# Optimization experiments

Hardware: AMD Instinct MI355X
Metric: run time of the kernel (lower is better)

The kernel has to match this reference:

```python
import jax, jax.numpy as jnp
import numpy as np

B, S, E, H = 4, 2048, 1024, 4
D = E // H  # head_dim = 256


def setup_inputs() -> dict:
    key = jax.random.key(0)
    ks = jax.random.split(key, 9)
    scale = 1.0 / np.sqrt(E)
    return {
        "hidden_states": jax.random.normal(ks[0], (B, S, E), jnp.float32),
        "Wq": jax.random.normal(ks[1], (E, E), jnp.float32) * scale,
        "Wk": jax.random.normal(ks[2], (E, E), jnp.float32) * scale,
        "Wv": jax.random.normal(ks[3], (E, E), jnp.float32) * scale,
        "Wo": jax.random.normal(ks[4], (E, E), jnp.float32) * scale,
        "bo": jax.random.normal(ks[5], (E,), jnp.float32) * 0.02,
        "betas": jax.random.normal(ks[6], (1, H, 1, 1), jnp.float32),
        "mem": jax.random.uniform(ks[7], (H, D, D), jnp.float32),
        "z": jax.random.uniform(ks[8], (H, D, 1), jnp.float32),
    }


def _split_heads(t):  # [B,S,E] -> [B,H,S,D]
    return t.reshape(B, S, H, D).transpose(0, 2, 1, 3)


def reference(hidden_states, Wq, Wk, Wv, Wo, bo, betas, mem, z):
    q = _split_heads(hidden_states @ Wq)  # [B,H,S,D]
    k = _split_heads(hidden_states @ Wk)
    v = _split_heads(hidden_states @ Wv)

    # linear-attention feature map (ELU + 1)
    sigma_q = jax.nn.elu(q) + 1.0
    sigma_k = jax.nn.elu(k) + 1.0

    # compressive-memory read: mem [H,D,D], z [H,D,1] broadcast over batch
    A_mem = (sigma_q @ mem) / (sigma_q @ z + 1e-6)  # [B,H,S,D]

    # standard causal softmax attention
    attn_weights = jnp.einsum("bhqd,bhkd->bhqk", q, k)
    causal = jnp.tril(jnp.ones((S, S), bool))
    mask_value = jnp.finfo(attn_weights.dtype).min
    attn_weights = jnp.where(causal, attn_weights, mask_value)
    attn_weights = jax.nn.softmax(attn_weights, axis=-1)
    attn_output = jnp.einsum("bhqk,bhkd->bhqd", attn_weights, v)

    # per-head sigmoid gate mixing memory read and local attention
    gate = jax.nn.sigmoid(betas)  # [1,H,1,1]
    attn_output = gate * A_mem + (1.0 - gate) * attn_output

    # memory update (delta rule)
    delta = (sigma_k @ mem) / (sigma_k @ z + 1e-6)  # [B,H,S,D]
    mem_new = mem + jnp.einsum("bhsd,bhse->bhde", sigma_k, v - delta)  # [B,H,D,D]
    z_new = z + sigma_k.sum(axis=-2, keepdims=True).transpose(0, 1, 3, 2)  # [B,H,D,1]

    out = attn_output.transpose(0, 2, 1, 3).reshape(B, S, E) @ Wo + bo
    return out, mem_new, z_new
```

## Files before the change

kernel.cpp:

```cpp
#include <hip/hip_runtime.h>
#include <math.h>

#define Bn 4
#define Sn 2048
#define En 1024
#define Hn 4
#define Dn 256

typedef _Float16 half8 __attribute__((ext_vector_type(8)));
typedef _Float16 half4v __attribute__((ext_vector_type(4)));
typedef float floatx4 __attribute__((ext_vector_type(4)));

#define MFMA16(a, b, c) __builtin_amdgcn_mfma_f32_16x16x32_f16((a), (b), (c), 0, 0, 0)

__device__ __forceinline__ float elup1(float x) {
    return x > 0.0f ? x + 1.0f : __expf(x);
}

__global__ __launch_bounds__(256) void trans_f32f16_k(
    const float* __restrict__ src, _Float16* __restrict__ dst, int R, int C) {
    __shared__ float T[64][65];
    const int tid = threadIdx.x;
    const int c0 = blockIdx.x * 64, r0 = blockIdx.y * 64;
    src += (size_t)blockIdx.z * R * C;
    dst += (size_t)blockIdx.z * R * C;
    {
        const int tr = tid >> 2, tc = (tid & 3) * 16;
        const float* s = src + (size_t)(r0 + tr) * C + c0 + tc;
        #pragma unroll
        for (int i = 0; i < 4; ++i) {
            float4 v = *(const float4*)(s + i * 4);
            T[tr][tc + i * 4 + 0] = v.x;
            T[tr][tc + i * 4 + 1] = v.y;
            T[tr][tc + i * 4 + 2] = v.z;
            T[tr][tc + i * 4 + 3] = v.w;
        }
    }
    __syncthreads();
    {
        const int cr = tid >> 2, rc = (tid & 3) * 16;
        half8 h0, h1;
        #pragma unroll
        for (int i = 0; i < 8; ++i) h0[i] = (_Float16)T[rc + i][cr];
        #pragma unroll
        for (int i = 0; i < 8; ++i) h1[i] = (_Float16)T[rc + 8 + i][cr];
        _Float16* d = dst + (size_t)(c0 + cr) * R + r0 + rc;
        *(half8*)d = h0;
        *(half8*)(d + 8) = h1;
    }
}

__global__ __launch_bounds__(256) void trans_h16_k(
    const _Float16* __restrict__ Vh, _Float16* __restrict__ Vtg) {
    __shared__ __align__(16) unsigned short T[64 * 72];
    const int tid = threadIdx.x;
    const int s0 = blockIdx.x * 64;
    const int e0 = blockIdx.y * 64;
    const int b = blockIdx.z;
    const int h = e0 >> 8, d0 = e0 & 255;
    {
        const int tr = tid >> 2, tc = (tid & 3) * 16;
        const _Float16* s = Vh + (size_t)(b * Sn + s0 + tr) * En + e0 + tc;
        _Float16* d = (_Float16*)T + tr * 72 + tc;
        *(half8*)d = *(const half8*)s;
        *(half8*)(d + 8) = *(const half8*)(s + 8);
    }
    __syncthreads();
    {
        const int dr = tid >> 2, sc = (tid & 3) * 16;
        const _Float16* Tp = (const _Float16*)T;
        half8 h0, h1;
        #pragma unroll
        for (int i = 0; i < 8; ++i) h0[i] = Tp[(sc + i) * 72 + dr];
        #pragma unroll
        for (int i = 0; i < 8; ++i) h1[i] = Tp[(sc + 8 + i) * 72 + dr];
        _Float16* d = Vtg + (size_t)((b * 4 + h) * 256 + d0 + dr) * (size_t)Sn + s0 + sc;
        *(half8*)d = h0;
        *(half8*)(d + 8) = h1;
    }
}

template <bool A32>
__global__ __launch_bounds__(256) void gemm16_k(
    const void* __restrict__ Ap, const _Float16* __restrict__ Bt,
    _Float16* __restrict__ C16, float* __restrict__ C32,
    const float* __restrict__ bias) {
    __shared__ __align__(16) unsigned short Ah[128 * 40];
    __shared__ __align__(16) unsigned short Bh[128 * 40];
    const int tid = threadIdx.x;
    const int lane = tid & 63, w = tid >> 6, quad = lane >> 4, l15 = lane & 15;
    const int bm = blockIdx.y * 128, bn = blockIdx.x * 128;
    floatx4 acc[2][8];
    #pragma unroll
    for (int mt = 0; mt < 2; ++mt)
        #pragma unroll
        for (int nt = 0; nt < 8; ++nt) acc[mt][nt] = (floatx4){0.f, 0.f, 0.f, 0.f};

    const int srow = tid >> 1, skoff = (tid & 1) * 16;
    const _Float16* bs = Bt + (size_t)(bn + srow) * 1024 + skoff;
    _Float16* ad = (_Float16*)Ah + srow * 40 + skoff;
    _Float16* bd = (_Float16*)Bh + srow * 40 + skoff;

    for (int k0 = 0; k0 < 1024; k0 += 32) {
        if (k0) __syncthreads();
        if constexpr (A32) {
            const float* as = (const float*)Ap + (size_t)(bm + srow) * 1024 + skoff + k0;
            half8 h0, h1;
            #pragma unroll
            for (int i = 0; i < 2; ++i) {
                float4 f0 = *(const float4*)(as + i * 8);
                float4 f1 = *(const float4*)(as + i * 8 + 4);
                half8* hp = i ? &h1 : &h0;
                (*hp)[0] = (_Float16)f0.x; (*hp)[1] = (_Float16)f0.y;
                (*hp)[2] = (_Float16)f0.z; (*hp)[3] = (_Float16)f0.w;
                (*hp)[4] = (_Float16)f1.x; (*hp)[5] = (_Float16)f1.y;
                (*hp)[6] = (_Float16)f1.z; (*hp)[7] = (_Float16)f1.w;
            }
            *(half8*)ad = h0;
            *(half8*)(ad + 8) = h1;
        } else {
            const _Float16* as = (const _Float16*)Ap + (size_t)(bm + srow) * 1024 + skoff + k0;
            *(half8*)ad = *(const half8*)as;
            *(half8*)(ad + 8) = *(const half8*)(as + 8);
        }
        *(half8*)bd = *(const half8*)(bs + k0);
        *(half8*)(bd + 8) = *(const half8*)(bs + k0 + 8);
        __syncthreads();
        half8 af0 = *(const half8*)((const _Float16*)Ah + (w * 32 + l15) * 40 + quad * 8);
        half8 af1 = *(const half8*)((const _Float16*)Ah + (w * 32 + 16 + l15) * 40 + quad * 8);
        #pragma unroll
        for (int nt = 0; nt < 8; ++nt) {
            half8 bf = *(const half8*)((const _Float16*)Bh + (nt * 16 + l15) * 40 + quad * 8);
            acc[0][nt] = MFMA16(af0, bf, acc[0][nt]);
            acc[1][nt] = MFMA16(af1, bf, acc[1][nt]);
        }
    }
    #pragma unroll
    for (int mt = 0; mt < 2; ++mt)
        #pragma unroll
        for (int nt = 0; nt < 8; ++nt)
            #pragma unroll
            for (int r = 0; r < 4; ++r) {
                const int row = bm + w * 32 + mt * 16 + quad * 4 + r;
                const int col = bn + nt * 16 + l15;
                if (C16)
                    C16[(size_t)row * 1024 + col] = (_Float16)acc[mt][nt][r];
                else
                    C32[(size_t)row * 1024 + col] = acc[mt][nt][r] + bias[col];
            }
}

__global__ __launch_bounds__(256, 3) void flash_gate_k(
    const _Float16* __restrict__ Qh, const _Float16* __restrict__ Khg,
    const _Float16* __restrict__ Vtg, const _Float16* __restrict__ memT,
    const float* __restrict__ zp, const float* __restrict__ betas,
    _Float16* __restrict__ Cmb, _Float16* __restrict__ Opart,
    float* __restrict__ mpart, float* __restrict__ lpart) {
    __shared__ __align__(16) unsigned short Ksh[32 * 264];
    __shared__ __align__(16) unsigned short Vt[256 * 40];
    __shared__ __align__(16) unsigned short Pb[64 * 40];

    const int tid = threadIdx.x;
    const int lane = tid & 63;
    const int w = tid >> 6;
    const int quad = lane >> 4;
    const int l15 = lane & 15;
    const int bx = blockIdx.x;
    const int bh = blockIdx.y;
    const int b = bh >> 2, h = bh & 3;

    int qt, kt0, kt1, unit;
    if (bx < 32) {
        qt = 31 - (bx >> 1);
        unit = bx & 1;
        kt0 = unit ? (qt + 1) : 0;
        kt1 = unit ? (2 * qt + 2) : (qt + 1);
    } else {
        qt = 15 - (bx - 32);
        unit = 0;
        kt0 = 0;
        kt1 = 2 * qt + 2;
    }
    const bool two = (bx < 32);
    const int q0 = qt * 64;

    const _Float16* Qrow = Qh + (size_t)(b * Sn + q0 + w * 16 + l15) * En + h * Dn;
    half8 qf[8];
    #pragma unroll
    for (int kc = 0; kc < 8; ++kc) qf[kc] = *(const half8*)(Qrow + kc * 32 + quad * 8);

    floatx4 acc[16];
    #pragma unroll
    for (int nt = 0; nt < 16; ++nt) acc[nt] = (floatx4){0.f, 0.f, 0.f, 0.f};

    const float gate = 1.0f / (1.0f + __expf(-betas[h]));
    const float omg = 1.0f - gate;
    _Float16* Cb = Cmb + (size_t)(b * Sn + q0 + w * 16) * En + h * Dn;
    _Float16* KshF = (_Float16*)Ksh;
    _Float16* VtF = (_Float16*)Vt;
    _Float16* PbF = (_Float16*)Pb;

    if (unit == 0) {
        float denp = 0.0f;
        const _Float16* memh = memT + (size_t)h * Dn * Dn;
        for (int dc = 0; dc < 8; ++dc) {
            __syncthreads();
            {
                const _Float16* src = memh + (size_t)tid * 256 + dc * 32;
                _Float16* dst = VtF + tid * 40;
                #pragma unroll
                for (int u = 0; u < 4; ++u) *(half8*)(dst + u * 8) = *(const half8*)(src + u * 8);
            }
            __syncthreads();
            half8 sv;
            const float* zb = zp + h * Dn + dc * 32 + quad * 8;
            #pragma unroll
            for (int j = 0; j < 8; ++j) {
                const float s = elup1((float)qf[dc][j]);
                sv[j] = (_Float16)s;
                denp += s * zb[j];
            }
            #pragma unroll
            for (int nt = 0; nt < 16; ++nt) {
                half8 bm = *(const half8*)(VtF + (nt * 16 + l15) * 40 + quad * 8);
                acc[nt] = MFMA16(sv, bm, acc[nt]);
            }
        }
        denp += __shfl_xor(denp, 16);
        denp += __shfl_xor(denp, 32);
        const float deninv = 1.0f / (denp + 1e-6f);
        float den4[4];
        #pragma unroll
        for (int r = 0; r < 4; ++r) den4[r] = __shfl(deninv, quad * 4 + r);
        #pragma unroll
        for (int nt = 0; nt < 16; ++nt)
            #pragma unroll
            for (int r = 0; r < 4; ++r) {
                Cb[(size_t)(quad * 4 + r) * En + nt * 16 + l15] =
                    (_Float16)(gate * acc[nt][r] * den4[r]);
                acc[nt][r] = 0.0f;
            }
    }

    const _Float16* Kbase = Khg + (size_t)(b * Sn) * En + h * Dn;
    const _Float16* Vtb = Vtg + (size_t)bh * 256 * (size_t)Sn;
    const _Float16* kptr = Kbase + (size_t)(kt0 * 32 + (tid >> 3)) * En + (tid & 7) * 32;
    const _Float16* vptr = Vtb + (size_t)tid * Sn + kt0 * 32;
    half8 kr[4], vr[4];
    #pragma unroll
    for (int u = 0; u < 4; ++u) {
        kr[u] = *(const half8*)(kptr + u * 8);
        vr[u] = *(const half8*)(vptr + u * 8);
    }

    float mold[4] = {-1e30f, -1e30f, -1e30f, -1e30f};
    float lsum[4] = {0.f, 0.f, 0.f, 0.f};
    float alpha[4];
    const int krow_off = (tid >> 3) * 264 + (tid & 7) * 32;

    for (int kt = kt0; kt < kt1; ++kt) {
        const int k0 = kt * 32;
        __syncthreads();
        #pragma unroll
        for (int u = 0; u < 4; ++u) {
            *(half8*)(KshF + krow_off + u * 8) = kr[u];
            *(half8*)(VtF + tid * 40 + u * 8) = vr[u];
        }
        __syncthreads();
        if (kt + 1 < kt1) {
            kptr += 32 * En;
            vptr += 32;
            #pragma unroll
            for (int u = 0; u < 4; ++u) {
                kr[u] = *(const half8*)(kptr + u * 8);
                vr[u] = *(const half8*)(vptr + u * 8);
            }
        }

        floatx4 S0 = (floatx4){0.f, 0.f, 0.f, 0.f};
        floatx4 S1 = (floatx4){0.f, 0.f, 0.f, 0.f};
        #pragma unroll
        for (int kc = 0; kc < 8; ++kc) {
            half8 kf0 = *(const half8*)(KshF + l15 * 264 + kc * 32 + quad * 8);
            half8 kf1 = *(const half8*)(KshF + (16 + l15) * 264 + kc * 32 + quad * 8);
            S0 = MFMA16(qf[kc], kf0, S0);
            S1 = MFMA16(qf[kc], kf1, S1);
        }
        if (kt >= 2 * qt) {
            #pragma unroll
            for (int r = 0; r < 4; ++r) {
                const int qg = q0 + w * 16 + quad * 4 + r;
                if (k0 + l15 > qg) S0[r] = -1e30f;
                if (k0 + 16 + l15 > qg) S1[r] = -1e30f;
            }
        }
        #pragma unroll
        for (int r = 0; r < 4; ++r) {
            float mx = fmaxf(S0[r], S1[r]);
            mx = fmaxf(mx, __shfl_xor(mx, 1));
            mx = fmaxf(mx, __shfl_xor(mx, 2));
            mx = fmaxf(mx, __shfl_xor(mx, 4));
            mx = fmaxf(mx, __shfl_xor(mx, 8));
            const float mnew = fmaxf(mold[r], mx);
            alpha[r] = __expf(mold[r] - mnew);
            mold[r] = mnew;
            const float p0 = __expf(S0[r] - mnew);
            const float p1 = __expf(S1[r] - mnew);
            float ps = p0 + p1;
            ps += __shfl_xor(ps, 1);
            ps += __shfl_xor(ps, 2);
            ps += __shfl_xor(ps, 4);
            ps += __shfl_xor(ps, 8);
            lsum[r] = lsum[r] * alpha[r] + ps;
            _Float16* pr = PbF + (w * 16 + quad * 4 + r) * 40;
            pr[l15] = (_Float16)p0;
            pr[16 + l15] = (_Float16)p1;
        }
        #pragma unroll
        for (int nt = 0; nt < 16; ++nt) {
            acc[nt][0] *= alpha[0];
            acc[nt][1] *= alpha[1];
            acc[nt][2] *= alpha[2];
            acc[nt][3] *= alpha[3];
        }
        __asm__ volatile("s_waitcnt lgkmcnt(0)" ::: "memory");
        half8 pf = *(const half8*)(PbF + (w * 16 + l15) * 40 + quad * 8);
        #pragma unroll
        for (int nt = 0; nt < 16; ++nt) {
            half8 vf = *(const half8*)(VtF + (nt * 16 + l15) * 40 + quad * 8);
            acc[nt] = MFMA16(pf, vf, acc[nt]);
        }
    }

    if (!two) {
        #pragma unroll
        for (int r = 0; r < 4; ++r) alpha[r] = omg / lsum[r];
        #pragma unroll
        for (int nt = 0; nt < 16; ++nt)
            #pragma unroll
            for (int r = 0; r < 4; ++r) {
                const size_t idx = (size_t)(quad * 4 + r) * En + nt * 16 + l15;
                Cb[idx] = (_Float16)((float)Cb[idx] + acc[nt][r] * alpha[r]);
            }
    } else {
        const int pidx = ((qt - 16) * 16 + bh) * 2 + unit;
        _Float16* Op = Opart + ((size_t)pidx * 64 + w * 16) * 256;
        #pragma unroll
        for (int nt = 0; nt < 16; ++nt)
            #pragma unroll
            for (int r = 0; r < 4; ++r)
                Op[(quad * 4 + r) * 256 + nt * 16 + l15] = (_Float16)acc[nt][r];
        if (l15 == 0) {
            #pragma unroll
            for (int r = 0; r < 4; ++r) {
                mpart[pidx * 64 + w * 16 + quad * 4 + r] = mold[r];
                lpart[pidx * 64 + w * 16 + quad * 4 + r] = lsum[r];
            }
        }
    }
}

__global__ __launch_bounds__(256) void merge_k(
    const _Float16* __restrict__ Opart, const float* __restrict__ mpart,
    const float* __restrict__ lpart, const float* __restrict__ betas,
    _Float16* __restrict__ Cmb) {
    const int qi = blockIdx.x;
    const int bh = blockIdx.y;
    const int b = bh >> 2, h = bh & 3;
    const int tid = threadIdx.x;
    const int idx = (qi * 16 + bh) * 2;
    const float gate = 1.0f / (1.0f + __expf(-betas[h]));
    const float omg = 1.0f - gate;
    const int rsub = tid >> 6;
    const int c0 = (tid & 63) * 4;
    const _Float16* O0 = Opart + (size_t)idx * 64 * 256;
    const _Float16* O1 = O0 + 64 * 256;
    const int q0 = (16 + qi) * 64;
    for (int chunk = 0; chunk < 16; ++chunk) {
        const int r = chunk * 4 + rsub;
        const float m0 = mpart[idx * 64 + r], l0 = lpart[idx * 64 + r];
        const float m1 = mpart[(idx + 1) * 64 + r], l1 = lpart[(idx + 1) * 64 + r];
        const float mm = fmaxf(m0, m1);
        const float s0 = __expf(m0 - mm), s1 = __expf(m1 - mm);
        const float rl = omg / (l0 * s0 + l1 * s1);
        half4v o0 = *(const half4v*)(O0 + r * 256 + c0);
        half4v o1 = *(const half4v*)(O1 + r * 256 + c0);
        _Float16* cp = Cmb + (size_t)(b * Sn + q0 + r) * En + h * Dn + c0;
        half4v cv = *(half4v*)cp;
        #pragma unroll
        for (int j = 0; j < 4; ++j)
            cv[j] = (_Float16)((float)cv[j] + ((float)o0[j] * s0 + (float)o1[j] * s1) * rl);
        *(half4v*)cp = cv;
    }
}

__global__ __launch_bounds__(256) void delta_v_k(
    const _Float16* __restrict__ Kg, _Float16* __restrict__ Vg,
    const float* __restrict__ memp, const float* __restrict__ zp) {
    __shared__ float SK[32][256];
    __shared__ float rden[32];
    const int tid = threadIdx.x;
    const int st = blockIdx.x;
    const int h = blockIdx.y;
    const int b = blockIdx.z;
    const int s0 = st * 32;
    const _Float16* Kb = Kg + (size_t)(b * Sn + s0) * En + h * Dn;
    _Float16* Vb = Vg + (size_t)(b * Sn + s0) * En + h * Dn;
    const float* memh = memp + (size_t)h * Dn * Dn;
    const float* zh = zp + (size_t)h * Dn;

    {
        const int lr = tid >> 3, ld = (tid & 7) * 32;
        const _Float16* kr = Kb + (size_t)lr * En + ld;
        #pragma unroll
        for (int u = 0; u < 4; ++u) {
            half8 k8 = *(const half8*)(kr + u * 8);
            #pragma unroll
            for (int j = 0; j < 8; ++j) SK[lr][ld + u * 8 + j] = elup1((float)k8[j]);
        }
    }
    __syncthreads();
    {
        const int r = tid >> 3;
        const int sl = (tid & 7) << 5;
        float part = 0.0f;
        #pragma unroll 8
        for (int d = 0; d < 32; ++d) part += SK[r][sl + d] * zh[sl + d];
        part += __shfl_down(part, 4);
        part += __shfl_down(part, 2);
        part += __shfl_down(part, 1);
        if ((tid & 7) == 0) rden[r] = 1.0f / (part + 1e-6f);
    }
    __syncthreads();
    const int c0 = (tid & 63) << 2;
    const int rb = tid >> 6;
    float dl[8][4] = {};
    for (int kk = 0; kk < Dn; ++kk) {
        const float4 m4 = *(const float4*)(memh + (size_t)kk * Dn + c0);
        #pragma unroll
        for (int k = 0; k < 8; ++k) {
            const float sk = SK[rb + 4 * k][kk];
            dl[k][0] += sk * m4.x;
            dl[k][1] += sk * m4.y;
            dl[k][2] += sk * m4.z;
            dl[k][3] += sk * m4.w;
        }
    }
    #pragma unroll
    for (int k = 0; k < 8; ++k) {
        const int r = rb + 4 * k;
        const float rd = rden[r];
        _Float16* vp = Vb + (size_t)r * En + c0;
        half4v v4 = *(half4v*)vp;
        #pragma unroll
        for (int j = 0; j < 4; ++j) v4[j] = (_Float16)((float)v4[j] - dl[k][j] * rd);
        *(half4v*)vp = v4;
    }
}

__global__ __launch_bounds__(256) void mem_update_k(
    const _Float16* __restrict__ Kg, const _Float16* __restrict__ U,
    const float* __restrict__ memp, float* __restrict__ mem_new) {
    __shared__ float As[16][64];
    __shared__ float Bs[16][64];
    const int tid = threadIdx.x;
    const int bn = blockIdx.x * 64;
    const int bm = blockIdx.y * 64;
    const int bh = blockIdx.z;
    const int b = bh >> 2;
    const int h = bh & 3;
    const _Float16* Kb = Kg + (size_t)b * Sn * En + h * Dn;
    const _Float16* Ub = U + (size_t)b * Sn * En + h * Dn;
    const int tr = tid >> 4, tc = tid & 15;
    const int lr = tid >> 4;
    const int lc = (tid & 15) << 2;
    float acc[4][4] = {};
    for (int s0 = 0; s0 < Sn; s0 += 16) {
        half4v a4 = *(const half4v*)(Kb + (size_t)(s0 + lr) * En + bm + lc);
        As[lr][lc + 0] = elup1((float)a4[0]);
        As[lr][lc + 1] = elup1((float)a4[1]);
        As[lr][lc + 2] = elup1((float)a4[2]);
        As[lr][lc + 3] = elup1((float)a4[3]);
        half4v b4 = *(const half4v*)(Ub + (size_t)(s0 + lr) * En + bn + lc);
        Bs[lr][lc + 0] = (float)b4[0];
        Bs[lr][lc + 1] = (float)b4[1];
        Bs[lr][lc + 2] = (float)b4[2];
        Bs[lr][lc + 3] = (float)b4[3];
        __syncthreads();
        #pragma unroll
        for (int kk = 0; kk < 16; ++kk) {
            float a[4], bb[4];
            #pragma unroll
            for (int i = 0; i < 4; ++i) a[i] = As[kk][tr * 4 + i];
            #pragma unroll
            for (int j = 0; j < 4; ++j) bb[j] = Bs[kk][tc * 4 + j];
            #pragma unroll
            for (int i = 0; i < 4; ++i)
                #pragma unroll
                for (int j = 0; j < 4; ++j)
                    acc[i][j] += a[i] * bb[j];
        }
        __syncthreads();
    }
    const float* memh = memp + (size_t)h * Dn * Dn;
    float* mout = mem_new + (size_t)bh * Dn * Dn;
    #pragma unroll
    for (int i = 0; i < 4; ++i) {
        const int dm = bm + tr * 4 + i;
        const float4 m4 = *(const float4*)(memh + (size_t)dm * Dn + bn + tc * 4);
        float4 r;
        r.x = m4.x + acc[i][0];
        r.y = m4.y + acc[i][1];
        r.z = m4.z + acc[i][2];
        r.w = m4.w + acc[i][3];
        *(float4*)(mout + (size_t)dm * Dn + bn + tc * 4) = r;
    }
}

__global__ __launch_bounds__(256) void znew_init_k(
    const float* __restrict__ zp, float* __restrict__ z_new) {
    const int bh = blockIdx.x;
    const int h = bh & 3;
    z_new[(size_t)bh * Dn + threadIdx.x] = zp[(size_t)h * Dn + threadIdx.x];
}

__global__ __launch_bounds__(256) void znew_acc_k(
    const _Float16* __restrict__ Kg, float* __restrict__ z_new) {
    const int bh = blockIdx.y;
    const int b = bh >> 2;
    const int h = bh & 3;
    const int s0 = blockIdx.x * 256;
    const _Float16* Kb = Kg + (size_t)(b * Sn + s0) * En + h * Dn;
    float acc = 0.0f;
    for (int s = 0; s < 256; ++s) acc += elup1((float)Kb[(size_t)s * En + threadIdx.x]);
    atomicAdd(&z_new[(size_t)bh * Dn + threadIdx.x], acc);
}

extern "C" void kernel_launch(void* const* d_in, const int* in_sizes, int n_in,
                              void* d_out, int out_size, void* d_ws, size_t ws_size,
                              hipStream_t stream) {
    const float* hidden = (const float*)d_in[0];
    const float* Wq = (const float*)d_in[1];
    const float* Wk = (const float*)d_in[2];
    const float* Wv = (const float*)d_in[3];
    const float* Wo = (const float*)d_in[4];
    const float* bo = (const float*)d_in[5];
    const float* betas = (const float*)d_in[6];
    const float* memp = (const float*)d_in[7];
    const float* zp = (const float*)d_in[8];

    float* out = (float*)d_out;
    float* mem_new = out + (size_t)Bn * Sn * En;
    float* z_new = mem_new + (size_t)Bn * Hn * Dn * Dn;

    const size_t BSE = (size_t)Bn * Sn * En;
    _Float16* p = (_Float16*)d_ws;
    _Float16* Qh = p;    p += BSE;
    _Float16* Kh = p;    p += BSE;
    _Float16* Vh = p;    p += BSE;
    _Float16* Vtg = p;   p += BSE;
    _Float16* Cmb = p;   p += BSE;
    _Float16* Opart = p; p += (size_t)512 * 64 * 256;
    _Float16* WqT = p;   p += (size_t)En * En;
    _Float16* WkT = p;   p += (size_t)En * En;
    _Float16* WvT = p;   p += (size_t)En * En;
    _Float16* WoT = p;   p += (size_t)En * En;
    _Float16* memT = p;  p += (size_t)Hn * Dn * Dn;
    float* fp = (float*)p;
    float* mpart = fp;   fp += 512 * 64;
    float* lpart = fp;   fp += 512 * 64;

    trans_f32f16_k<<<dim3(16, 16, 1), 256, 0, stream>>>(Wq, WqT, En, En);
    trans_f32f16_k<<<dim3(16, 16, 1), 256, 0, stream>>>(Wk, WkT, En, En);
    trans_f32f16_k<<<dim3(16, 16, 1), 256, 0, stream>>>(Wv, WvT, En, En);
    trans_f32f16_k<<<dim3(16, 16, 1), 256, 0, stream>>>(Wo, WoT, En, En);
    trans_f32f16_k<<<dim3(4, 4, 4), 256, 0, stream>>>(memp, memT, Dn, Dn);

    gemm16_k<true><<<dim3(8, 64), 256, 0, stream>>>(hidden, WqT, Qh, nullptr, nullptr);
    gemm16_k<true><<<dim3(8, 64), 256, 0, stream>>>(hidden, WkT, Kh, nullptr, nullptr);
    gemm16_k<true><<<dim3(8, 64), 256, 0, stream>>>(hidden, WvT, Vh, nullptr, nullptr);

    trans_h16_k<<<dim3(32, 16, 4), 256, 0, stream>>>(Vh, Vtg);

    flash_gate_k<<<dim3(48, 16), 256, 0, stream>>>(
        Qh, Kh, Vtg, memT, zp, betas, Cmb, Opart, mpart, lpart);
    merge_k<<<dim3(16, 16), 256, 0, stream>>>(Opart, mpart, lpart, betas, Cmb);

    delta_v_k<<<dim3(64, 4, 4), 256, 0, stream>>>(Kh, Vh, memp, zp);
    mem_update_k<<<dim3(4, 4, 16), 256, 0, stream>>>(Kh, Vh, memp, mem_new);

    znew_init_k<<<16, 256, 0, stream>>>(zp, z_new);
    znew_acc_k<<<dim3(8, 16), 256, 0, stream>>>(Kh, z_new);

    gemm16_k<false><<<dim3(8, 64), 256, 0, stream>>>(Cmb, WoT, nullptr, out, bo);
}
```

Before: 651.5 us.

## Fuse QKV GEMM, move delta/memory update to MFMA, drop LDS staging in flash kernel

The hidden state is converted to fp16 once, and a single fused QKV GEMM with 64x64 warp tiles and a K-step of 64 scatters its output into Q, K and V. The flash kernel now reads K, V and mem fragments straight from global memory instead of staging them in LDS. It computes the row sum through an extra MFMA against a ones vector and skips the rescale when the running max does not change. The scalar fp32 delta-rule and memory-update kernels are replaced by MFMA kernels working on transposed sigma_k and V-minus-delta buffers. Uncoalesced direct global reads in the attention loop could increase memory latency.

Result: slower. 711.4 us (+9.2%).

```diff
diff --git a/kernel.cpp b/kernel.cpp
--- a/kernel.cpp
+++ b/kernel.cpp
@@ -15,6 +15,18 @@
 
 __device__ __forceinline__ float elup1(float x) {
     return x > 0.0f ? x + 1.0f : __expf(x);
+}
+
+__global__ void cvt_h_k(const float* __restrict__ src, _Float16* __restrict__ dst, int n4) {
+    int idx = blockIdx.x * 256 + threadIdx.x;
+    const int stride = gridDim.x * 256;
+    for (; idx < n4; idx += stride) {
+        float4 v = ((const float4*)src)[idx];
+        half4v o;
+        o[0] = (_Float16)v.x; o[1] = (_Float16)v.y;
+        o[2] = (_Float16)v.z; o[3] = (_Float16)v.w;
+        ((half4v*)dst)[idx] = o;
+    }
 }
 
 __global__ __launch_bounds__(256) void trans_f32f16_k(
@@ -80,73 +92,70 @@
     }
 }
 
-template <bool A32>
-__global__ __launch_bounds__(256) void gemm16_k(
-    const void* __restrict__ Ap, const _Float16* __restrict__ Bt,
-    _Float16* __restrict__ C16, float* __restrict__ C32,
-    const float* __restrict__ bias) {
-    __shared__ __align__(16) unsigned short Ah[128 * 40];
-    __shared__ __align__(16) unsigned short Bh[128 * 40];
+template <bool OUT32>
+__global__ __launch_bounds__(256) void gemm_fused_k(
+    const _Float16* __restrict__ A, const _Float16* __restrict__ Bt,
+    _Float16* __restrict__ Qo, _Float16* __restrict__ Ko, _Float16* __restrict__ Vo,
+    float* __restrict__ C32, const float* __restrict__ bias) {
+    __shared__ __align__(16) unsigned short Ah[128 * 72];
+    __shared__ __align__(16) unsigned short Bh[128 * 72];
     const int tid = threadIdx.x;
     const int lane = tid & 63, w = tid >> 6, quad = lane >> 4, l15 = lane & 15;
     const int bm = blockIdx.y * 128, bn = blockIdx.x * 128;
-    floatx4 acc[2][8];
-    #pragma unroll
-    for (int mt = 0; mt < 2; ++mt)
-        #pragma unroll
-        for (int nt = 0; nt < 8; ++nt) acc[mt][nt] = (floatx4){0.f, 0.f, 0.f, 0.f};
-
-    const int srow = tid >> 1, skoff = (tid & 1) * 16;
+    const int wr = (w >> 1) * 64, wc = (w & 1) * 64;
+    floatx4 acc[4][4];
+    #pragma unroll
+    for (int mt = 0; mt < 4; ++mt)
+        #pragma unroll
+        for (int nt = 0; nt < 4; ++nt) acc[mt][nt] = (floatx4){0.f, 0.f, 0.f, 0.f};
+
+    const int srow = tid >> 1, skoff = (tid & 1) * 32;
+    const _Float16* as = A + (size_t)(bm + srow) * 1024 + skoff;
     const _Float16* bs = Bt + (size_t)(bn + srow) * 1024 + skoff;
-    _Float16* ad = (_Float16*)Ah + srow * 40 + skoff;
-    _Float16* bd = (_Float16*)Bh + srow * 40 + skoff;
-
-    for (int k0 = 0; k0 < 1024; k0 += 32) {
+    _Float16* ad = (_Float16*)Ah + srow * 72 + skoff;
+    _Float16* bd = (_Float16*)Bh + srow * 72 + skoff;
+    const _Float16* AhF = (const _Float16*)Ah;
+    const _Float16* BhF = (const _Float16*)Bh;
+
+    for (int k0 = 0; k0 < 1024; k0 += 64) {
         if (k0) __syncthreads();
-        if constexpr (A32) {
-            const float* as = (const float*)Ap + (size_t)(bm + srow) * 1024 + skoff + k0;
-            half8 h0, h1;
-            #pragma unroll
-            for (int i = 0; i < 2; ++i) {
-                float4 f0 = *(const float4*)(as + i * 8);
-                float4 f1 = *(const float4*)(as + i * 8 + 4);
-                half8* hp = i ? &h1 : &h0;
-                (*hp)[0] = (_Float16)f0.x; (*hp)[1] = (_Float16)f0.y;
-                (*hp)[2] = (_Float16)f0.z; (*hp)[3] = (_Float16)f0.w;
-                (*hp)[4] = (_Float16)f1.x; (*hp)[5] = (_Float16)f1.y;
-                (*hp)[6] = (_Float16)f1.z; (*hp)[7] = (_Float16)f1.w;
-            }
-            *(half8*)ad = h0;
-            *(half8*)(ad + 8) = h1;
-        } else {
-            const _Float16* as = (const _Float16*)Ap + (size_t)(bm + srow) * 1024 + skoff + k0;
-            *(half8*)ad = *(const half8*)as;
-            *(half8*)(ad + 8) = *(const half8*)(as + 8);
-        }
-        *(half8*)bd = *(const half8*)(bs + k0);
-        *(half8*)(bd + 8) = *(const half8*)(bs + k0 + 8);
+        #pragma unroll
+        for (int u = 0; u < 4; ++u) {
+            *(half8*)(ad + u * 8) = *(const half8*)(as + k0 + u * 8);
+            *(half8*)(bd + u * 8) = *(const half8*)(bs + k0 + u * 8);
+        }
         __syncthreads();
-        half8 af0 = *(const half8*)((const _Float16*)Ah + (w * 32 + l15) * 40 + quad * 8);
-        half8 af1 = *(const half8*)((const _Float16*)Ah + (w * 32 + 16 + l15) * 40 + quad * 8);
-        #pragma unroll
-        for (int nt = 0; nt < 8; ++nt) {
-            half8 bf = *(const half8*)((const _Float16*)Bh + (nt * 16 + l15) * 40 + quad * 8);
-            acc[0][nt] = MFMA16(af0, bf, acc[0][nt]);
-            acc[1][nt] = MFMA16(af1, bf, acc[1][nt]);
-        }
-    }
-    #pragma unroll
-    for (int mt = 0; mt < 2; ++mt)
-        #pragma unroll
-        for (int nt = 0; nt < 8; ++nt)
+        #pragma unroll
+        for (int ks = 0; ks < 2; ++ks) {
+            half8 af[4], bf[4];
+            #pragma unroll
+            for (int mt = 0; mt < 4; ++mt)
+                af[mt] = *(const half8*)(AhF + (wr + mt * 16 + l15) * 72 + ks * 32 + quad * 8);
+            #pragma unroll
+            for (int nt = 0; nt < 4; ++nt)
+                bf[nt] = *(const half8*)(BhF + (wc + nt * 16 + l15) * 72 + ks * 32 + quad * 8);
+            #pragma unroll
+            for (int mt = 0; mt < 4; ++mt)
+                #pragma unroll
+                for (int nt = 0; nt < 4; ++nt)
+                    acc[mt][nt] = MFMA16(af[mt], bf[nt], acc[mt][nt]);
+        }
+    }
+    #pragma unroll
+    for (int mt = 0; mt < 4; ++mt)
+        #pragma unroll
+        for (int nt = 0; nt < 4; ++nt)
             #pragma unroll
             for (int r = 0; r < 4; ++r) {
-                const int row = bm + w * 32 + mt * 16 + quad * 4 + r;
-                const int col = bn + nt * 16 + l15;
-                if (C16)
-                    C16[(size_t)row * 1024 + col] = (_Float16)acc[mt][nt][r];
-                else
+                const int row = bm + wr + mt * 16 + quad * 4 + r;
+                const int col = bn + wc + nt * 16 + l15;
+                if constexpr (OUT32) {
                     C32[(size_t)row * 1024 + col] = acc[mt][nt][r] + bias[col];
+                } else {
+                    const int m = col >> 10, c = col & 1023;
+                    _Float16* dst = (m == 0) ? Qo : ((m == 1) ? Ko : Vo);
+                    dst[(size_t)row * 1024 + c] = (_Float16)acc[mt][nt][r];
+                }
             }
 }
 
@@ -156,17 +165,11 @@
     const float* __restrict__ zp, const float* __restrict__ betas,
     _Float16* __restrict__ Cmb, _Float16* __restrict__ Opart,
     float* __restrict__ mpart, float* __restrict__ lpart) {
-    __shared__ __align__(16) unsigned short Ksh[32 * 264];
-    __shared__ __align__(16) unsigned short Vt[256 * 40];
-    __shared__ __align__(16) unsigned short Pb[64 * 40];
-
+    __shared__ __align__(16) unsigned short Pb[4 * 16 * 40];
     const int tid = threadIdx.x;
     const int lane = tid & 63;
-    const int w = tid >> 6;
-    const int quad = lane >> 4;
-    const int l15 = lane & 15;
-    const int bx = blockIdx.x;
-    const int bh = blockIdx.y;
+    const int w = tid >> 6, quad = lane >> 4, l15 = lane & 15;
+    const int bx = blockIdx.x, bh = blockIdx.y;
     const int b = bh >> 2, h = bh & 3;
 
     int qt, kt0, kt1, unit;
@@ -189,29 +192,22 @@
     #pragma unroll
     for (int kc = 0; kc < 8; ++kc) qf[kc] = *(const half8*)(Qrow + kc * 32 + quad * 8);
 
-    floatx4 acc[16];
-    #pragma unroll
-    for (int nt = 0; nt < 16; ++nt) acc[nt] = (floatx4){0.f, 0.f, 0.f, 0.f};
+    floatx4 acc[17];
+    #pragma unroll
+    for (int nt = 0; nt < 17; ++nt) acc[nt] = (floatx4){0.f, 0.f, 0.f, 0.f};
+    half8 ones;
+    #pragma unroll
+    for (int j = 0; j < 8; ++j) ones[j] = (_Float16)1.0f;
 
     const float gate = 1.0f / (1.0f + __expf(-betas[h]));
     const float omg = 1.0f - gate;
     _Float16* Cb = Cmb + (size_t)(b * Sn + q0 + w * 16) * En + h * Dn;
-    _Float16* KshF = (_Float16*)Ksh;
-    _Float16* VtF = (_Float16*)Vt;
     _Float16* PbF = (_Float16*)Pb;
 
     if (unit == 0) {
         float denp = 0.0f;
-        const _Float16* memh = memT + (size_t)h * Dn * Dn;
+        const _Float16* memh = memT + (size_t)h * Dn * Dn + (size_t)l15 * Dn + quad * 8;
         for (int dc = 0; dc < 8; ++dc) {
-            __syncthreads();
-            {
-                const _Float16* src = memh + (size_t)tid * 256 + dc * 32;
-                _Float16* dst = VtF + tid * 40;
-                #pragma unroll
-                for (int u = 0; u < 4; ++u) *(half8*)(dst + u * 8) = *(const half8*)(src + u * 8);
-            }
-            __syncthreads();
             half8 sv;
             const float* zb = zp + h * Dn + dc * 32 + quad * 8;
             #pragma unroll
@@ -222,8 +218,8 @@
             }
             #pragma unroll
             for (int nt = 0; nt < 16; ++nt) {
-                half8 bm = *(const half8*)(VtF + (nt * 16 + l15) * 40 + quad * 8);
-                acc[nt] = MFMA16(sv, bm, acc[nt]);
+                half8 bmf = *(const half8*)(memh + (size_t)(nt * 16) * Dn + dc * 32);
+                acc[nt] = MFMA16(sv, bmf, acc[nt]);
             }
         }
         denp += __shfl_xor(denp, 16);
@@ -242,51 +238,25 @@
             }
     }
 
-    const _Float16* Kbase = Khg + (size_t)(b * Sn) * En + h * Dn;
-    const _Float16* Vtb = Vtg + (size_t)bh * 256 * (size_t)Sn;
-    const _Float16* kptr = Kbase + (size_t)(kt0 * 32 + (tid >> 3)) * En + (tid & 7) * 32;
-    const _Float16* vptr = Vtb + (size_t)tid * Sn + kt0 * 32;
-    half8 kr[4], vr[4];
-    #pragma unroll
-    for (int u = 0; u < 4; ++u) {
-        kr[u] = *(const half8*)(kptr + u * 8);
-        vr[u] = *(const half8*)(vptr + u * 8);
-    }
-
+    const _Float16* kb0 = Khg + (size_t)(b * Sn + kt0 * 32 + l15) * En + h * Dn + quad * 8;
+    const _Float16* kb1 = kb0 + (size_t)16 * En;
+    const _Float16* vb = Vtg + (size_t)(bh * 256 + l15) * Sn + kt0 * 32 + quad * 8;
     float mold[4] = {-1e30f, -1e30f, -1e30f, -1e30f};
-    float lsum[4] = {0.f, 0.f, 0.f, 0.f};
-    float alpha[4];
-    const int krow_off = (tid >> 3) * 264 + (tid & 7) * 32;
 
     for (int kt = kt0; kt < kt1; ++kt) {
-        const int k0 = kt * 32;
-        __syncthreads();
-        #pragma unroll
-        for (int u = 0; u < 4; ++u) {
-            *(half8*)(KshF + krow_off + u * 8) = kr[u];
-            *(half8*)(VtF + tid * 40 + u * 8) = vr[u];
-        }
-        __syncthreads();
-        if (kt + 1 < kt1) {
-            kptr += 32 * En;
-            vptr += 32;
-            #pragma unroll
-            for (int u = 0; u < 4; ++u) {
-                kr[u] = *(const half8*)(kptr + u * 8);
-                vr[u] = *(const half8*)(vptr + u * 8);
-            }
-        }
-
         floatx4 S0 = (floatx4){0.f, 0.f, 0.f, 0.f};
         floatx4 S1 = (floatx4){0.f, 0.f, 0.f, 0.f};
         #pragma unroll
         for (int kc = 0; kc < 8; ++kc) {
-            half8 kf0 = *(const half8*)(KshF + l15 * 264 + kc * 32 + quad * 8);
-            half8 kf1 = *(const half8*)(KshF + (16 + l15) * 264 + kc * 32 + quad * 8);
+            half8 kf0 = *(const half8*)(kb0 + kc * 32);
+            half8 kf1 = *(const half8*)(kb1 + kc * 32);
             S0 = MFMA16(qf[kc], kf0, S0);
             S1 = MFMA16(qf[kc], kf1, S1);
         }
+        kb0 += (size_t)32 * En;
+        kb1 += (size_t)32 * En;
         if (kt >= 2 * qt) {
+            const int k0 = kt * 32;
             #pragma unroll
             for (int r = 0; r < 4; ++r) {
                 const int qg = q0 + w * 16 + quad * 4 + r;
@@ -294,6 +264,8 @@
                 if (k0 + 16 + l15 > qg) S1[r] = -1e30f;
             }
         }
+        float alpha[4];
+        bool nr = true;
         #pragma unroll
         for (int r = 0; r < 4; ++r) {
             float mx = fmaxf(S0[r], S1[r]);
@@ -303,45 +275,44 @@
             mx = fmaxf(mx, __shfl_xor(mx, 8));
             const float mnew = fmaxf(mold[r], mx);
             alpha[r] = __expf(mold[r] - mnew);
+            nr = nr && (mnew == mold[r]);
             mold[r] = mnew;
             const float p0 = __expf(S0[r] - mnew);
             const float p1 = __expf(S1[r] - mnew);
-            float ps = p0 + p1;
-            ps += __shfl_xor(ps, 1);
-            ps += __shfl_xor(ps, 2);
-            ps += __shfl_xor(ps, 4);
-            ps += __shfl_xor(ps, 8);
-            lsum[r] = lsum[r] * alpha[r] + ps;
             _Float16* pr = PbF + (w * 16 + quad * 4 + r) * 40;
             pr[l15] = (_Float16)p0;
             pr[16 + l15] = (_Float16)p1;
         }
-        #pragma unroll
-        for (int nt = 0; nt < 16; ++nt) {
-            acc[nt][0] *= alpha[0];
-            acc[nt][1] *= alpha[1];
-            acc[nt][2] *= alpha[2];
-            acc[nt][3] *= alpha[3];
+        if (__ballot(nr) != 0xFFFFFFFFFFFFFFFFull) {
+            #pragma unroll
+            for (int nt = 0; nt < 17; ++nt) {
+                acc[nt][0] *= alpha[0];
+                acc[nt][1] *= alpha[1];
+                acc[nt][2] *= alpha[2];
+                acc[nt][3] *= alpha[3];
+            }
         }
         __asm__ volatile("s_waitcnt lgkmcnt(0)" ::: "memory");
         half8 pf = *(const half8*)(PbF + (w * 16 + l15) * 40 + quad * 8);
         #pragma unroll
         for (int nt = 0; nt < 16; ++nt) {
-            half8 vf = *(const half8*)(VtF + (nt * 16 + l15) * 40 + quad * 8);
+            half8 vf = *(const half8*)(vb + (size_t)(nt * 16) * Sn);
             acc[nt] = MFMA16(pf, vf, acc[nt]);
         }
+        acc[16] = MFMA16(pf, ones, acc[16]);
+        vb += 32;
     }
 
     if (!two) {
         #pragma unroll
-        for (int r = 0; r < 4; ++r) alpha[r] = omg / lsum[r];
-        #pragma unroll
-        for (int nt = 0; nt < 16; ++nt)
-            #pragma unroll
-            for (int r = 0; r < 4; ++r) {
+        for (int r = 0; r < 4; ++r) {
+            const float sc = omg / acc[16][r];
+            #pragma unroll
+            for (int nt = 0; nt < 16; ++nt) {
                 const size_t idx = (size_t)(quad * 4 + r) * En + nt * 16 + l15;
-                Cb[idx] = (_Float16)((float)Cb[idx] + acc[nt][r] * alpha[r]);
-            }
+                Cb[idx] = (_Float16)((float)Cb[idx] + acc[nt][r] * sc);
+            }
+        }
     } else {
         const int pidx = ((qt - 16) * 16 + bh) * 2 + unit;
         _Float16* Op = Opart + ((size_t)pidx * 64 + w * 16) * 256;
@@ -354,7 +325,7 @@
             #pragma unroll
             for (int r = 0; r < 4; ++r) {
                 mpart[pidx * 64 + w * 16 + quad * 4 + r] = mold[r];
-                lpart[pidx * 64 + w * 16 + quad * 4 + r] = lsum[r];
+                lpart[pidx * 64 + w * 16 + quad * 4 + r] = acc[16][r];
             }
         }
     }
@@ -394,127 +365,133 @@
     }
 }
 
-__global__ __launch_bounds__(256) void delta_v_k(
-    const _Float16* __restrict__ Kg, _Float16* __restrict__ Vg,
-    const float* __restrict__ memp, const float* __restrict__ zp) {
-    __shared__ float SK[32][256];
-    __shared__ float rden[32];
-    const int tid = threadIdx.x;
-    const int st = blockIdx.x;
-    const int h = blockIdx.y;
-    const int b = blockIdx.z;
-    const int s0 = st * 32;
-    const _Float16* Kb = Kg + (size_t)(b * Sn + s0) * En + h * Dn;
-    _Float16* Vb = Vg + (size_t)(b * Sn + s0) * En + h * Dn;
-    const float* memh = memp + (size_t)h * Dn * Dn;
-    const float* zh = zp + (size_t)h * Dn;
-
-    {
-        const int lr = tid >> 3, ld = (tid & 7) * 32;
-        const _Float16* kr = Kb + (size_t)lr * En + ld;
-        #pragma unroll
-        for (int u = 0; u < 4; ++u) {
-            half8 k8 = *(const half8*)(kr + u * 8);
-            #pragma unroll
-            for (int j = 0; j < 8; ++j) SK[lr][ld + u * 8 + j] = elup1((float)k8[j]);
-        }
-    }
+__global__ __launch_bounds__(256) void delta_ut_k(
+    const _Float16* __restrict__ Kg, _Float16* __restrict__ Vtg,
+    _Float16* __restrict__ SkT, const _Float16* __restrict__ memT,
+    const float* __restrict__ zp) {
+    __shared__ __align__(16) unsigned short L[256 * 72];
+    const int tid = threadIdx.x;
+    const int lane = tid & 63;
+    const int w = tid >> 6, quad = lane >> 4, l15 = lane & 15;
+    const int s0 = blockIdx.x * 64;
+    const int bh = blockIdx.y;
+    const int b = bh >> 2, h = bh & 3;
+    _Float16* Lf = (_Float16*)L;
+
+    const _Float16* Krow = Kg + (size_t)(b * Sn + s0 + w * 16 + l15) * En + h * Dn;
+    half8 skf[8];
+    float denp = 0.0f;
+    #pragma unroll
+    for (int kc = 0; kc < 8; ++kc) {
+        half8 kv = *(const half8*)(Krow + kc * 32 + quad * 8);
+        const float* zb = zp + h * Dn + kc * 32 + quad * 8;
+        #pragma unroll
+        for (int j = 0; j < 8; ++j) {
+            const float s = elup1((float)kv[j]);
+            skf[kc][j] = (_Float16)s;
+            denp += s * zb[j];
+        }
+    }
+    denp += __shfl_xor(denp, 16);
+    denp += __shfl_xor(denp, 32);
+    const float deninv = 1.0f / (denp + 1e-6f);
+    float den4[4];
+    #pragma unroll
+    for (int r = 0; r < 4; ++r) den4[r] = __shfl(deninv, quad * 4 + r);
+
+    floatx4 acc[16];
+    #pragma unroll
+    for (int nt = 0; nt < 16; ++nt) acc[nt] = (floatx4){0.f, 0.f, 0.f, 0.f};
+    const _Float16* memh = memT + (size_t)h * Dn * Dn + (size_t)l15 * Dn + quad * 8;
+    #pragma unroll
+    for (int kc = 0; kc < 8; ++kc)
+        #pragma unroll
+        for (int nt = 0; nt < 16; ++nt) {
+            half8 bmf = *(const half8*)(memh + (size_t)(nt * 16) * Dn + kc * 32);
+            acc[nt] = MFMA16(skf[kc], bmf, acc[nt]);
+        }
+
+    #pragma unroll
+    for (int nt = 0; nt < 16; ++nt)
+        #pragma unroll
+        for (int r = 0; r < 4; ++r)
+            Lf[(nt * 16 + l15) * 72 + w * 16 + quad * 4 + r] =
+                (_Float16)(acc[nt][r] * den4[r]);
     __syncthreads();
     {
-        const int r = tid >> 3;
-        const int sl = (tid & 7) << 5;
-        float part = 0.0f;
-        #pragma unroll 8
-        for (int d = 0; d < 32; ++d) part += SK[r][sl + d] * zh[sl + d];
-        part += __shfl_down(part, 4);
-        part += __shfl_down(part, 2);
-        part += __shfl_down(part, 1);
-        if ((tid & 7) == 0) rden[r] = 1.0f / (part + 1e-6f);
+        _Float16* Vrow = Vtg + (size_t)(bh * 256 + tid) * Sn + s0;
+        #pragma unroll
+        for (int u = 0; u < 8; ++u) {
+            half8 v = *(const half8*)(Vrow + u * 8);
+            half8 d = *(const half8*)(Lf + tid * 72 + u * 8);
+            #pragma unroll
+            for (int j = 0; j < 8; ++j) v[j] = v[j] - d[j];
+            *(half8*)(Vrow + u * 8) = v;
+        }
     }
     __syncthreads();
-    const int c0 = (tid & 63) << 2;
-    const int rb = tid >> 6;
-    float dl[8][4] = {};
-    for (int kk = 0; kk < Dn; ++kk) {
-        const float4 m4 = *(const float4*)(memh + (size_t)kk * Dn + c0);
-        #pragma unroll
-        for (int k = 0; k < 8; ++k) {
-            const float sk = SK[rb + 4 * k][kk];
-            dl[k][0] += sk * m4.x;
-            dl[k][1] += sk * m4.y;
-            dl[k][2] += sk * m4.z;
-            dl[k][3] += sk * m4.w;
-        }
-    }
-    #pragma unroll
-    for (int k = 0; k < 8; ++k) {
-        const int r = rb + 4 * k;
-        const float rd = rden[r];
-        _Float16* vp = Vb + (size_t)r * En + c0;
-        half4v v4 = *(half4v*)vp;
-        #pragma unroll
-        for (int j = 0; j < 4; ++j) v4[j] = (_Float16)((float)v4[j] - dl[k][j] * rd);
-        *(half4v*)vp = v4;
-    }
-}
-
-__global__ __launch_bounds__(256) void mem_update_k(
-    const _Float16* __restrict__ Kg, const _Float16* __restrict__ U,
+    #pragma unroll
+    for (int kc = 0; kc < 8; ++kc)
+        #pragma unroll
+        for (int j = 0; j < 8; ++j)
+            Lf[(kc * 32 + quad * 8 + j) * 72 + w * 16 + l15] = skf[kc][j];
+    __syncthreads();
+    {
+        _Float16* Srow = SkT + (size_t)(bh * 256 + tid) * Sn + s0;
+        #pragma unroll
+        for (int u = 0; u < 8; ++u)
+            *(half8*)(Srow + u * 8) = *(const half8*)(Lf + tid * 72 + u * 8);
+    }
+}
+
+__global__ __launch_bounds__(256) void memupd_k(
+    const _Float16* __restrict__ SkT, const _Float16* __restrict__ UT,
     const float* __restrict__ memp, float* __restrict__ mem_new) {
-    __shared__ float As[16][64];
-    __shared__ float Bs[16][64];
-    const int tid = threadIdx.x;
-    const int bn = blockIdx.x * 64;
-    const int bm = blockIdx.y * 64;
-    const int bh = blockIdx.z;
-    const int b = bh >> 2;
-    const int h = bh & 3;
-    const _Float16* Kb = Kg + (size_t)b * Sn * En + h * Dn;
-    const _Float16* Ub = U + (size_t)b * Sn * En + h * Dn;
-    const int tr = tid >> 4, tc = tid & 15;
-    const int lr = tid >> 4;
-    const int lc = (tid & 15) << 2;
-    float acc[4][4] = {};
-    for (int s0 = 0; s0 < Sn; s0 += 16) {
-        half4v a4 = *(const half4v*)(Kb + (size_t)(s0 + lr) * En + bm + lc);
-        As[lr][lc + 0] = elup1((float)a4[0]);
-        As[lr][lc + 1] = elup1((float)a4[1]);
-        As[lr][lc + 2] = elup1((float)a4[2]);
-        As[lr][lc + 3] = elup1((float)a4[3]);
-        half4v b4 = *(const half4v*)(Ub + (size_t)(s0 + lr) * En + bn + lc);
-        Bs[lr][lc + 0] = (float)b4[0];
-        Bs[lr][lc + 1] = (float)b4[1];
-        Bs[lr][lc + 2] = (float)b4[2];
-        Bs[lr][lc + 3] = (float)b4[3];
+    __shared__ __align__(16) unsigned short Ah[64 * 72];
+    __shared__ __align__(16) unsigned short Bh[64 * 72];
+    const int tid = threadIdx.x;
+    const int lane = tid & 63, w = tid >> 6, quad = lane >> 4, l15 = lane & 15;
+    const int bn = blockIdx.x * 64, bm = blockIdx.y * 64;
+    const int bh = blockIdx.z, h = bh & 3;
+    const _Float16* Ab = SkT + (size_t)(bh * 256 + bm) * Sn;
+    const _Float16* Bb = UT + (size_t)(bh * 256 + bn) * Sn;
+    floatx4 acc[4];
+    #pragma unroll
+    for (int nt = 0; nt < 4; ++nt) acc[nt] = (floatx4){0.f, 0.f, 0.f, 0.f};
+
+    const int srow = tid >> 2, skoff = (tid & 3) * 16;
+    _Float16* ad = (_Float16*)Ah + srow * 72 + skoff;
+    _Float16* bd = (_Float16*)Bh + srow * 72 + skoff;
+    const _Float16* AhF = (const _Float16*)Ah;
+    const _Float16* BhF = (const _Float16*)Bh;
+
+    for (int k0 = 0; k0 < Sn; k0 += 64) {
+        if (k0) __syncthreads();
+        *(half8*)ad = *(const half8*)(Ab + (size_t)srow * Sn + k0 + skoff);
+        *(half8*)(ad + 8) = *(const half8*)(Ab + (size_t)srow * Sn + k0 + skoff + 8);
+        *(half8*)bd = *(const half8*)(Bb + (size_t)srow * Sn + k0 + skoff);
+        *(half8*)(bd + 8) = *(const half8*)(Bb + (size_t)srow * Sn + k0 + skoff + 8);
         __syncthreads();
         #pragma unroll
-        for (int kk = 0; kk < 16; ++kk) {
-            float a[4], bb[4];
-            #pragma unroll
-            for (int i = 0; i < 4; ++i) a[i] = As[kk][tr * 4 + i];
-            #pragma unroll
-            for (int j = 0; j < 4; ++j) bb[j] = Bs[kk][tc * 4 + j];
-            #pragma unroll
-            for (int i = 0; i < 4; ++i)
-                #pragma unroll
-                for (int j = 0; j < 4; ++j)
-                    acc[i][j] += a[i] * bb[j];
-        }
-        __syncthreads();
-    }
-    const float* memh = memp + (size_t)h * Dn * Dn;
-    float* mout = mem_new + (size_t)bh * Dn * Dn;
-    #pragma unroll
-    for (int i = 0; i < 4; ++i) {
-        const int dm = bm + tr * 4 + i;
-        const float4 m4 = *(const float4*)(memh + (size_t)dm * Dn + bn + tc * 4);
-        float4 r;
-        r.x = m4.x + acc[i][0];
-        r.y = m4.y + acc[i][1];
-        r.z = m4.z + acc[i][2];
-        r.w = m4.w + acc[i][3];
-        *(float4*)(mout + (size_t)dm * Dn + bn + tc * 4) = r;
-    }
+        for (int ks = 0; ks < 2; ++ks) {
+            half8 af = *(const half8*)(AhF + (w * 16 + l15) * 72 + ks * 32 + quad * 8);
+            #pragma unroll
+            for (int nt = 0; nt < 4; ++nt) {
+                half8 bf = *(const half8*)(BhF + (nt * 16 + l15) * 72 + ks * 32 + quad * 8);
+                acc[nt] = MFMA16(af, bf, acc[nt]);
+            }
+        }
+    }
+    const float* mh = memp + (size_t)h * Dn * Dn;
+    float* mo = mem_new + (size_t)bh * Dn * Dn;
+    #pragma unroll
+    for (int nt = 0; nt < 4; ++nt)
+        #pragma unroll
+        for (int r = 0; r < 4; ++r) {
+            const int d = bm + w * 16 + quad * 4 + r;
+            const int e = bn + nt * 16 + l15;
+            mo[(size_t)d * Dn + e] = mh[(size_t)d * Dn + e] + acc[nt][r];
+        }
 }
 
 __global__ __launch_bounds__(256) void znew_init_k(
@@ -560,25 +537,25 @@
     _Float16* Vh = p;    p += BSE;
     _Float16* Vtg = p;   p += BSE;
     _Float16* Cmb = p;   p += BSE;
-    _Float16* Opart = p; p += (size_t)512 * 64 * 256;
-    _Float16* WqT = p;   p += (size_t)En * En;
-    _Float16* WkT = p;   p += (size_t)En * En;
-    _Float16* WvT = p;   p += (size_t)En * En;
+    _Float16* Opart = p; p += BSE;
+    _Float16* hh = p;    p += BSE;
+    _Float16* WqT = p;   p += (size_t)3 * En * En;
     _Float16* WoT = p;   p += (size_t)En * En;
     _Float16* memT = p;  p += (size_t)Hn * Dn * Dn;
     float* fp = (float*)p;
     float* mpart = fp;   fp += 512 * 64;
     float* lpart = fp;   fp += 512 * 64;
+    _Float16* SkT = hh;
 
     trans_f32f16_k<<<dim3(16, 16, 1), 256, 0, stream>>>(Wq, WqT, En, En);
-    trans_f32f16_k<<<dim3(16, 16, 1), 256, 0, stream>>>(Wk, WkT, En, En);
-    trans_f32f16_k<<<dim3(16, 16, 1), 256, 0, stream>>>(Wv, WvT, En, En);
+    trans_f32f16_k<<<dim3(16, 16, 1), 256, 0, stream>>>(Wk, WqT + (size_t)En * En, En, En);
+    trans_f32f16_k<<<dim3(16, 16, 1), 256, 0, stream>>>(Wv, WqT + (size_t)2 * En * En, En, En);
     trans_f32f16_k<<<dim3(16, 16, 1), 256, 0, stream>>>(Wo, WoT, En, En);
     trans_f32f16_k<<<dim3(4, 4, 4), 256, 0, stream>>>(memp, memT, Dn, Dn);
-
-    gemm16_k<true><<<dim3(8, 64), 256, 0, stream>>>(hidden, WqT, Qh, nullptr, nullptr);
-    gemm16_k<true><<<dim3(8, 64), 256, 0, stream>>>(hidden, WkT, Kh, nullptr, nullptr);
-    gemm16_k<true><<<dim3(8, 64), 256, 0, stream>>>(hidden, WvT, Vh, nullptr, nullptr);
+    cvt_h_k<<<2048, 256, 0, stream>>>(hidden, hh, (int)(BSE / 4));
+
+    gemm_fused_k<false><<<dim3(24, 64), 256, 0, stream>>>(
+        hh, WqT, Qh, Kh, Vh, nullptr, nullptr);
 
     trans_h16_k<<<dim3(32, 16, 4), 256, 0, stream>>>(Vh, Vtg);
 
@@ -586,11 +563,12 @@
         Qh, Kh, Vtg, memT, zp, betas, Cmb, Opart, mpart, lpart);
     merge_k<<<dim3(16, 16), 256, 0, stream>>>(Opart, mpart, lpart, betas, Cmb);
 
-    delta_v_k<<<dim3(64, 4, 4), 256, 0, stream>>>(Kh, Vh, memp, zp);
-    mem_update_k<<<dim3(4, 4, 16), 256, 0, stream>>>(Kh, Vh, memp, mem_new);
+    delta_ut_k<<<dim3(32, 16), 256, 0, stream>>>(Kh, Vtg, SkT, memT, zp);
+    memupd_k<<<dim3(4, 4, 16), 256, 0, stream>>>(SkT, Vtg, memp, mem_new);
 
     znew_init_k<<<16, 256, 0, stream>>>(zp, z_new);
     znew_acc_k<<<dim3(8, 16), 256, 0, stream>>>(Kh, z_new);
 
-    gemm16_k<false><<<dim3(8, 64), 256, 0, stream>>>(Cmb, WoT, nullptr, out, bo);
-}
+    gemm_fused_k<true><<<dim3(8, 64), 256, 0, stream>>>(
+        Cmb, WoT, nullptr, nullptr, nullptr, out, bo);
+}
```
